# Optimization experiments

Measured on AMD Instinct MI355X. Metric: run time of the kernel, lower is better.

Reference implementation:

```python
import jax, jax.numpy as jnp
import numpy as np

B, IN, OUT = 4096, 1024, 1024

def setup_inputs() -> dict:
    key = jax.random.key(0)
    k1, k2 = jax.random.split(key)
    xs = jax.random.uniform(k1, (B, IN), dtype=jnp.float32)          # fuzzy truth values in [0,1]
    weights = jax.random.normal(k2, (IN, OUT), dtype=jnp.float32)    # raw weights (pre-sigmoid)
    return {"xs": xs, "weights": weights}


def reference(xs, weights):
    # get_weights(): sigmoid maps raw params to valid fuzzy booleans in [0,1]
    w = jax.nn.sigmoid(weights)                                       # [IN, OUT]
    # Weighted Lukasiewicz conjunction:
    #   out[b, j] = max(0, 1 - sum_i w[i, j] * (1 - xs[b, i]))
    # Broadcast+reduce collapses to a single GEMM over in_features.
    s = jnp.einsum('bi,io->bo', 1.0 - xs, w)                          # [B, OUT]
    return jnp.maximum(1.0 - s, 0.0)
```

## Files before the change

kernel.cpp:

```cpp
#include <hip/hip_runtime.h>
#include <hip/hip_bf16.h>
#include <math.h>


constexpr int Bsz = 4096;
constexpr int IN  = 1024;
constexpr int OUT = 1024;

constexpr int BM = 128;
constexpr int BN = 64;
constexpr int BK = 64;

typedef __attribute__((ext_vector_type(8))) short bf16x8;
typedef __attribute__((ext_vector_type(4))) float f32x4;

__device__ inline unsigned short f2bf(float f) {
    union { float f; unsigned u; } c{f};
    unsigned lsb = (c.u >> 16) & 1u;
    unsigned r = c.u + 0x7fffu + lsb;
    return (unsigned short)(r >> 16);
}

__global__ void prep_fused(const float* __restrict__ xs, const float* __restrict__ w,
                           unsigned short* __restrict__ A, unsigned short* __restrict__ WT) {
    if (blockIdx.x < 2048) {
        int idx = (blockIdx.x * 256 + threadIdx.x) * 2;
        float4 v0 = ((const float4*)xs)[idx];
        float4 v1 = ((const float4*)xs)[idx + 1];
        ushort4 o0, o1;
        o0.x = f2bf(1.0f - v0.x); o0.y = f2bf(1.0f - v0.y);
        o0.z = f2bf(1.0f - v0.z); o0.w = f2bf(1.0f - v0.w);
        o1.x = f2bf(1.0f - v1.x); o1.y = f2bf(1.0f - v1.y);
        o1.z = f2bf(1.0f - v1.z); o1.w = f2bf(1.0f - v1.w);
        ((ushort4*)A)[idx]     = o0;
        ((ushort4*)A)[idx + 1] = o1;
    } else {
        __shared__ unsigned short t[32][33];
        int wblk = blockIdx.x - 2048;
        int o0 = (wblk & 31) * 32, i0 = (wblk >> 5) * 32;
        int tx = threadIdx.x & 31, ty = threadIdx.x >> 5;
#pragma unroll
        for (int r = 0; r < 4; ++r) {
            int row = ty + r * 8;
            float v = w[(size_t)(i0 + row) * OUT + o0 + tx];
            float s = 1.0f / (1.0f + __expf(-v));
            t[row][tx] = f2bf(s);
        }
        __syncthreads();
#pragma unroll
        for (int r = 0; r < 4; ++r) {
            int row = ty + r * 8;
            WT[(size_t)(o0 + row) * IN + i0 + tx] = t[tx][row];
        }
    }
}

__device__ inline void load_lds16(const unsigned short* g, unsigned short* l) {
    __builtin_amdgcn_global_load_lds(
        (const __attribute__((address_space(1))) void*)g,
        (__attribute__((address_space(3))) void*)l, 16, 0, 0);
}

__global__ __launch_bounds__(256) void gemm_fuzzy(const unsigned short* __restrict__ A,
                                                  const unsigned short* __restrict__ Bt,
                                                  float* __restrict__ C) {
    __shared__ unsigned short As[2][BM * BK];
    __shared__ unsigned short Bs[2][BN * BK];

    const int tid  = threadIdx.x;
    const int lane = tid & 63;
    const int wave = tid >> 6;
    const int quad = lane >> 4;
    const int l16  = lane & 15;
    const int wm   = (wave >> 1) * 64;
    const int wn   = (wave & 1) * 32;
    const int bm   = blockIdx.y * BM;
    const int bn   = blockIdx.x * BN;

    const unsigned short* AgSrc[4];
    unsigned short* AgDst[4][2];
#pragma unroll
    for (int r = 0; r < 4; ++r) {
        int c = tid + r * 256;
        int m = c >> 3;
        int gkb = (((c & 7) ^ (m & 7)) << 3);
        AgSrc[r] = A + (size_t)(bm + m) * IN + gkb;
        AgDst[r][0] = &As[0][c << 3];
        AgDst[r][1] = &As[1][c << 3];
    }
    const unsigned short* BgSrc[2];
    unsigned short* BgDst[2][2];
#pragma unroll
    for (int r = 0; r < 2; ++r) {
        int c = tid + r * 256;
        int n = c >> 3;
        int gkb = (((c & 7) ^ (n & 7)) << 3);
        BgSrc[r] = Bt + (size_t)(bn + n) * IN + gkb;
        BgDst[r][0] = &Bs[0][c << 3];
        BgDst[r][1] = &Bs[1][c << 3];
    }

    f32x4 acc[4][2] = {};

#pragma unroll
    for (int r = 0; r < 4; ++r) load_lds16(AgSrc[r], AgDst[r][0]);
#pragma unroll
    for (int r = 0; r < 2; ++r) load_lds16(BgSrc[r], BgDst[r][0]);

    const int NITER = IN / BK;
    for (int i = 0; i < NITER; ++i) {
        __syncthreads();

        if (i + 1 < NITER) {
            int k0 = (i + 1) * BK;
            int nb = (i + 1) & 1;
#pragma unroll
            for (int r = 0; r < 4; ++r) load_lds16(AgSrc[r] + k0, AgDst[r][nb]);
#pragma unroll
            for (int r = 0; r < 2; ++r) load_lds16(BgSrc[r] + k0, BgDst[r][nb]);
        }

        const unsigned short* as = As[i & 1];
        const unsigned short* bs = Bs[i & 1];
#pragma unroll
        for (int s = 0; s < 2; ++s) {
            int koff = ((((s << 2) | quad) ^ (l16 & 7)) << 3);
            bf16x8 af[4], bfr[2];
#pragma unroll
            for (int mt = 0; mt < 4; ++mt)
                af[mt] = *(const bf16x8*)&as[(wm + mt * 16 + l16) * BK + koff];
#pragma unroll
            for (int nt = 0; nt < 2; ++nt)
                bfr[nt] = *(const bf16x8*)&bs[(wn + nt * 16 + l16) * BK + koff];
#pragma unroll
            for (int mt = 0; mt < 4; ++mt)
#pragma unroll
                for (int nt = 0; nt < 2; ++nt)
                    acc[mt][nt] = __builtin_amdgcn_mfma_f32_16x16x32_bf16(
                        af[mt], bfr[nt], acc[mt][nt], 0, 0, 0);
        }
    }

#pragma unroll
    for (int mt = 0; mt < 4; ++mt) {
#pragma unroll
        for (int nt = 0; nt < 2; ++nt) {
#pragma unroll
            for (int r = 0; r < 4; ++r) {
                int row = bm + wm + mt * 16 + quad * 4 + r;
                int col = bn + wn + nt * 16 + l16;
                float v = 1.0f - acc[mt][nt][r];
                C[(size_t)row * OUT + col] = fmaxf(v, 0.0f);
            }
        }
    }
}

extern "C" void kernel_launch(void* const* d_in, const int* in_sizes, int n_in,
                              void* d_out, int out_size, void* d_ws, size_t ws_size,
                              hipStream_t stream) {
    const float* xs = (const float*)d_in[0];
    const float* wt = (const float*)d_in[1];
    float* out = (float*)d_out;

    unsigned short* A  = (unsigned short*)d_ws;
    unsigned short* WT = (unsigned short*)((char*)d_ws + (size_t)Bsz * IN * 2);

    prep_fused<<<2048 + 1024, 256, 0, stream>>>(xs, wt, A, WT);
    gemm_fuzzy<<<dim3(OUT / BN, Bsz / BM), 256, 0, stream>>>(A, WT, out);
}
```

Before: 89.76 us.

## Halve GEMM M-tile and switch to register-staged double-buffered prefetch

Shrinks the block tile from 128x64 to 64x64, doubling the grid, and sets launch bounds to allow 4 blocks per CU. The direct global-to-LDS loads are replaced by a register-staged pipeline that prefetches two K-steps ahead into registers and writes to the other LDS buffer after the MFMAs. The aim is more occupancy and better hiding of load latency. In exchange, each block reuses less data, global traffic for B goes up, and every iteration now costs extra VGPRs and LDS store instructions.

```diff
diff --git a/kernel.cpp b/kernel.cpp
--- a/kernel.cpp
+++ b/kernel.cpp
@@ -7,7 +7,7 @@
 constexpr int IN  = 1024;
 constexpr int OUT = 1024;
 
-constexpr int BM = 128;
+constexpr int BM = 64;
 constexpr int BN = 64;
 constexpr int BK = 64;
 
@@ -55,15 +55,9 @@
     }
 }
 
-__device__ inline void load_lds16(const unsigned short* g, unsigned short* l) {
-    __builtin_amdgcn_global_load_lds(
-        (const __attribute__((address_space(1))) void*)g,
-        (__attribute__((address_space(3))) void*)l, 16, 0, 0);
-}
-
-__global__ __launch_bounds__(256) void gemm_fuzzy(const unsigned short* __restrict__ A,
-                                                  const unsigned short* __restrict__ Bt,
-                                                  float* __restrict__ C) {
+__global__ __launch_bounds__(256, 4) void gemm_fuzzy(const unsigned short* __restrict__ A,
+                                                     const unsigned short* __restrict__ Bt,
+                                                     float* __restrict__ C) {
     __shared__ unsigned short As[2][BM * BK];
     __shared__ unsigned short Bs[2][BN * BK];
 
@@ -72,77 +66,78 @@
     const int wave = tid >> 6;
     const int quad = lane >> 4;
     const int l16  = lane & 15;
-    const int wm   = (wave >> 1) * 64;
+    const int wm   = (wave >> 1) * 32;
     const int wn   = (wave & 1) * 32;
     const int bm   = blockIdx.y * BM;
     const int bn   = blockIdx.x * BN;
 
-    const unsigned short* AgSrc[4];
-    unsigned short* AgDst[4][2];
-#pragma unroll
-    for (int r = 0; r < 4; ++r) {
-        int c = tid + r * 256;
-        int m = c >> 3;
-        int gkb = (((c & 7) ^ (m & 7)) << 3);
-        AgSrc[r] = A + (size_t)(bm + m) * IN + gkb;
-        AgDst[r][0] = &As[0][c << 3];
-        AgDst[r][1] = &As[1][c << 3];
-    }
-    const unsigned short* BgSrc[2];
-    unsigned short* BgDst[2][2];
-#pragma unroll
-    for (int r = 0; r < 2; ++r) {
-        int c = tid + r * 256;
-        int n = c >> 3;
-        int gkb = (((c & 7) ^ (n & 7)) << 3);
-        BgSrc[r] = Bt + (size_t)(bn + n) * IN + gkb;
-        BgDst[r][0] = &Bs[0][c << 3];
-        BgDst[r][1] = &Bs[1][c << 3];
-    }
+    const int c0 = tid, c1 = tid + 256;
+    const int ar0 = c0 >> 3, ak0 = c0 & 7;
+    const int ar1 = c1 >> 3, ak1 = c1 & 7;
+    const unsigned short* Ag0 = A  + (size_t)(bm + ar0) * IN + ak0 * 8;
+    const unsigned short* Ag1 = A  + (size_t)(bm + ar1) * IN + ak1 * 8;
+    const unsigned short* Bg0 = Bt + (size_t)(bn + ar0) * IN + ak0 * 8;
+    const unsigned short* Bg1 = Bt + (size_t)(bn + ar1) * IN + ak1 * 8;
+    const int ad0 = ((c0 & ~7) | (ak0 ^ (ar0 & 7))) * 8;
+    const int ad1 = ((c1 & ~7) | (ak1 ^ (ar1 & 7))) * 8;
 
-    f32x4 acc[4][2] = {};
+    bf16x8 rA[2][2], rB[2][2];
+
+    rA[0][0] = *(const bf16x8*)Ag0; rA[0][1] = *(const bf16x8*)Ag1;
+    rB[0][0] = *(const bf16x8*)Bg0; rB[0][1] = *(const bf16x8*)Bg1;
+    *(bf16x8*)&As[0][ad0] = rA[0][0]; *(bf16x8*)&As[0][ad1] = rA[0][1];
+    *(bf16x8*)&Bs[0][ad0] = rB[0][0]; *(bf16x8*)&Bs[0][ad1] = rB[0][1];
+    rA[1][0] = *(const bf16x8*)(Ag0 + BK); rA[1][1] = *(const bf16x8*)(Ag1 + BK);
+    rB[1][0] = *(const bf16x8*)(Bg0 + BK); rB[1][1] = *(const bf16x8*)(Bg1 + BK);
+    __syncthreads();
+
+    f32x4 acc[2][2] = {};
+    const int NIT = IN / BK;
 
 #pragma unroll
-    for (int r = 0; r < 4; ++r) load_lds16(AgSrc[r], AgDst[r][0]);
-#pragma unroll
-    for (int r = 0; r < 2; ++r) load_lds16(BgSrc[r], BgDst[r][0]);
-
-    const int NITER = IN / BK;
-    for (int i = 0; i < NITER; ++i) {
-        __syncthreads();
-
-        if (i + 1 < NITER) {
-            int k0 = (i + 1) * BK;
-            int nb = (i + 1) & 1;
-#pragma unroll
-            for (int r = 0; r < 4; ++r) load_lds16(AgSrc[r] + k0, AgDst[r][nb]);
-#pragma unroll
-            for (int r = 0; r < 2; ++r) load_lds16(BgSrc[r] + k0, BgDst[r][nb]);
+    for (int i = 0; i < NIT; ++i) {
+        if (i + 2 < NIT) {
+            int k0 = (i + 2) * BK;
+            rA[i & 1][0] = *(const bf16x8*)(Ag0 + k0);
+            rA[i & 1][1] = *(const bf16x8*)(Ag1 + k0);
+            rB[i & 1][0] = *(const bf16x8*)(Bg0 + k0);
+            rB[i & 1][1] = *(const bf16x8*)(Bg1 + k0);
         }
 
         const unsigned short* as = As[i & 1];
         const unsigned short* bs = Bs[i & 1];
 #pragma unroll
         for (int s = 0; s < 2; ++s) {
-            int koff = ((((s << 2) | quad) ^ (l16 & 7)) << 3);
-            bf16x8 af[4], bfr[2];
+            const int kc = s * 4 + quad;
+            bf16x8 af[2], bfr[2];
 #pragma unroll
-            for (int mt = 0; mt < 4; ++mt)
-                af[mt] = *(const bf16x8*)&as[(wm + mt * 16 + l16) * BK + koff];
+            for (int mt = 0; mt < 2; ++mt) {
+                int row = wm + mt * 16 + l16;
+                af[mt] = *(const bf16x8*)&as[(row * 8 + (kc ^ (row & 7))) * 8];
+            }
 #pragma unroll
-            for (int nt = 0; nt < 2; ++nt)
-                bfr[nt] = *(const bf16x8*)&bs[(wn + nt * 16 + l16) * BK + koff];
+            for (int nt = 0; nt < 2; ++nt) {
+                int row = wn + nt * 16 + l16;
+                bfr[nt] = *(const bf16x8*)&bs[(row * 8 + (kc ^ (row & 7))) * 8];
+            }
 #pragma unroll
-            for (int mt = 0; mt < 4; ++mt)
+            for (int mt = 0; mt < 2; ++mt)
 #pragma unroll
                 for (int nt = 0; nt < 2; ++nt)
                     acc[mt][nt] = __builtin_amdgcn_mfma_f32_16x16x32_bf16(
                         af[mt], bfr[nt], acc[mt][nt], 0, 0, 0);
         }
+
+        if (i + 1 < NIT) {
+            int nb = (i + 1) & 1;
+            *(bf16x8*)&As[nb][ad0] = rA[nb][0]; *(bf16x8*)&As[nb][ad1] = rA[nb][1];
+            *(bf16x8*)&Bs[nb][ad0] = rB[nb][0]; *(bf16x8*)&Bs[nb][ad1] = rB[nb][1];
+        }
+        __syncthreads();
     }
 
 #pragma unroll
-    for (int mt = 0; mt < 4; ++mt) {
+    for (int mt = 0; mt < 2; ++mt) {
 #pragma unroll
         for (int nt = 0; nt < 2; ++nt) {
 #pragma unroll
```

Result: no change. 88.38 us (-1.5%).
